# Performance work log

Hardware: AMD Instinct MI355X
Metric: run time of the kernel (lower is better)

The kernel has to match this reference:

```python
import jax, jax.numpy as jnp
import numpy as np

B, T, C = 2, 2048, 1024
NUM_HEADS, QK_LEN, V_LEN = 16, 64, 64


def setup_inputs() -> dict:
    key = jax.random.key(0)
    ks = jax.random.split(key, 11)
    s = 0.02
    return {
        "Q": jax.random.normal(ks[0], (B, T, C), jnp.float32),
        "K": jax.random.normal(ks[1], (B, T, C), jnp.float32),
        "V": jax.random.normal(ks[2], (B, T, C), jnp.float32),
        # Linear weights stored as (in, out); y = x @ W + b
        "Wq": jax.random.normal(ks[3], (C, NUM_HEADS * QK_LEN), jnp.float32) * s,
        "bq": jnp.zeros((NUM_HEADS * QK_LEN,), jnp.float32),
        "Wk": jax.random.normal(ks[4], (C, NUM_HEADS * QK_LEN), jnp.float32) * s,
        "bk": jnp.zeros((NUM_HEADS * QK_LEN,), jnp.float32),
        "Wv": jax.random.normal(ks[5], (C, NUM_HEADS * V_LEN), jnp.float32) * s,
        "bv": jnp.zeros((NUM_HEADS * V_LEN,), jnp.float32),
        "Wo": jax.random.normal(ks[6], (NUM_HEADS * V_LEN, C), jnp.float32) * s,
        "bo": jnp.zeros((C,), jnp.float32),
    }


def _split_heads(x, n_heads, d):
    b, t, _ = x.shape
    return x.reshape(b, t, n_heads, d).transpose(0, 2, 1, 3)  # (B,H,T,d)


def reference(Q, K, V, Wq, bq, Wk, bk, Wv, bv, Wo, bo):
    q = _split_heads(Q @ Wq + bq, NUM_HEADS, QK_LEN)   # (B,H,T,dk)
    k = _split_heads(K @ Wk + bk, NUM_HEADS, QK_LEN)   # (B,H,T,dk)
    v = _split_heads(V @ Wv + bv, NUM_HEADS, V_LEN)    # (B,H,T,dv)

    scale = 1.0 / jnp.sqrt(jnp.asarray(QK_LEN, q.dtype))
    scores = jnp.einsum("bhqd,bhkd->bhqk", q, k) * scale  # (B,H,T,T)
    attn = jax.nn.softmax(scores, axis=-1)
    out = jnp.einsum("bhqk,bhkd->bhqd", attn, v)           # (B,H,T,dv)

    out = out.transpose(0, 2, 1, 3).reshape(Q.shape[0], Q.shape[1], NUM_HEADS * V_LEN)
    return out @ Wo + bo
```

## Files before the change

### kernel.cpp

```cpp
#include <hip/hip_runtime.h>
#include <hip/hip_bf16.h>
#include <math.h>

constexpr int B = 2, T = 2048, C = 1024, H = 16, D = 64;
constexpr int M = B * T;
constexpr float SCALE_L2E = 0.125f * 1.4426950408889634f;

typedef __attribute__((ext_vector_type(8))) short s16x8;
typedef __attribute__((ext_vector_type(4))) short s16x4;
typedef __attribute__((ext_vector_type(4))) float fv4;

typedef unsigned short ushort_t;

static __device__ __forceinline__ ushort_t f2bf(float x) {
    union { float f; unsigned u; } c; c.f = x;
    unsigned u = c.u + 0x7FFFu + ((c.u >> 16) & 1u);
    return (ushort_t)(u >> 16);
}

#define GLDS(gp, lp) __builtin_amdgcn_global_load_lds( \
    (const __attribute__((address_space(1))) void*)(gp), \
    (__attribute__((address_space(3))) void*)(lp), 16, 0, 0)

__global__ __launch_bounds__(256) void convert_qkv(
    const float* __restrict__ Q, const float* __restrict__ K,
    const float* __restrict__ V, ushort_t* __restrict__ dst)
{
    size_t e = ((size_t)blockIdx.x * 256 + threadIdx.x) * 8;
    const float* src;
    size_t base;
    if (e < (size_t)M * C)          { src = Q; base = 0; }
    else if (e < 2 * (size_t)M * C) { src = K; base = (size_t)M * C; }
    else                            { src = V; base = 2 * (size_t)M * C; }
    const float* p = src + (e - base);
    float4 a = *(const float4*)p;
    float4 b = *(const float4*)(p + 4);
    union { s16x8 v; ushort_t u[8]; } o;
    o.u[0] = f2bf(a.x); o.u[1] = f2bf(a.y); o.u[2] = f2bf(a.z); o.u[3] = f2bf(a.w);
    o.u[4] = f2bf(b.x); o.u[5] = f2bf(b.y); o.u[6] = f2bf(b.z); o.u[7] = f2bf(b.w);
    *(s16x8*)(dst + e) = o.v;
}

__global__ __launch_bounds__(256) void transpose_w(
    const float* __restrict__ W0, const float* __restrict__ W1,
    const float* __restrict__ W2, const float* __restrict__ W3,
    ushort_t* __restrict__ Wt)
{
    const int s = blockIdx.z;
    const float* W = (s == 0) ? W0 : (s == 1) ? W1 : (s == 2) ? W2 : W3;
    const int k0 = blockIdx.x * 64, n0 = blockIdx.y * 64;
    __shared__ ushort_t tile[64][72];
    const int tid = threadIdx.x;
#pragma unroll
    for (int it = 0; it < 4; it++) {
        int f = it * 256 + tid;
        int r = f >> 4, c4 = (f & 15) * 4;
        float4 x = *(const float4*)(W + (size_t)(k0 + r) * C + n0 + c4);
        tile[r][c4 + 0] = f2bf(x.x);
        tile[r][c4 + 1] = f2bf(x.y);
        tile[r][c4 + 2] = f2bf(x.z);
        tile[r][c4 + 3] = f2bf(x.w);
    }
    __syncthreads();
#pragma unroll
    for (int it = 0; it < 4; it++) {
        int f = it * 256 + tid;
        int rr = f >> 4, c4 = (f & 15) * 4;
        union { s16x4 v; ushort_t u[4]; } u;
#pragma unroll
        for (int j = 0; j < 4; j++) u.u[j] = tile[c4 + j][rr];
        *(s16x4*)(Wt + (size_t)(s * 1024 + n0 + rr) * 1024 + k0 + c4) = u.v;
    }
}

__global__ __launch_bounds__(256) void transpose_v(
    const ushort_t* __restrict__ vw, ushort_t* __restrict__ vt)
{
    __shared__ ushort_t tile[64][72];
    const int tid = threadIdx.x;
    const int t0 = blockIdx.x * 64;
    const int bh = blockIdx.y;
    const ushort_t* src = vw + ((size_t)bh * T + t0) * D;
#pragma unroll
    for (int it = 0; it < 2; it++) {
        int f = it * 256 + tid;
        int row = f >> 3, c8 = (f & 7) * 8;
        *(s16x8*)&tile[row][c8] = *(const s16x8*)(src + (size_t)row * D + c8);
    }
    __syncthreads();
    ushort_t* dst = vt + (size_t)bh * D * T + t0;
#pragma unroll
    for (int it = 0; it < 4; it++) {
        int f = it * 256 + tid;
        int d = f >> 4, t4 = (f & 15) * 4;
        union { s16x4 v; ushort_t u[4]; } u;
#pragma unroll
        for (int j = 0; j < 4; j++) u.u[j] = tile[t4 + j][d];
        *(s16x4*)(dst + (size_t)d * T + t4) = u.v;
    }
}

__global__ __launch_bounds__(256) void gemm_qkv(
    const ushort_t* __restrict__ qkv, const ushort_t* __restrict__ Wt,
    const float* __restrict__ bq, const float* __restrict__ bk,
    const float* __restrict__ bv,
    ushort_t* __restrict__ qw, ushort_t* __restrict__ kw,
    ushort_t* __restrict__ vw)
{
    __shared__ ushort_t As[2][128 * 32];
    __shared__ ushort_t Bs[2][128 * 32];

    const int tid = threadIdx.x;
    const int w = tid >> 6, lane = tid & 63;
    const int quad = lane >> 4, lc = lane & 15;
    const int wm = w & 1, wn = w >> 1;

    const int nt = blockIdx.x;
    const int m0 = blockIdx.y * 128;
    const int s = nt >> 3;
    const int nsec0 = (nt & 7) * 128;

    const ushort_t* Abase = qkv + (size_t)s * M * C;
    const ushort_t* Btbase = Wt + (size_t)nt * 128 * 1024;

    const int srow = (w << 4) + (lane >> 2);
    const int ske  = (lane & 3) * 8;

    fv4 acc[4][4] = {};

    auto stage = [&](int k0, int buf) {
#pragma unroll
        for (int i = 0; i < 2; i++) {
            int row = i * 64 + srow;
            GLDS(Abase + (size_t)(m0 + row) * 1024 + k0 + ske,
                 As[buf] + i * 2048 + w * 512);
            GLDS(Btbase + (size_t)row * 1024 + k0 + ske,
                 Bs[buf] + i * 2048 + w * 512);
        }
    };

    stage(0, 0);
    __syncthreads();

    for (int k0 = 0; k0 < 1024; k0 += 32) {
        const int cur = (k0 >> 5) & 1;
        if (k0 + 32 < 1024) stage(k0 + 32, cur ^ 1);

        s16x8 af[4], bf[4];
#pragma unroll
        for (int ms = 0; ms < 4; ms++)
            af[ms] = *(const s16x8*)(As[cur] + (wm * 64 + ms * 16 + lc) * 32 + quad * 8);
#pragma unroll
        for (int ns = 0; ns < 4; ns++)
            bf[ns] = *(const s16x8*)(Bs[cur] + (wn * 64 + ns * 16 + lc) * 32 + quad * 8);
#pragma unroll
        for (int ms = 0; ms < 4; ms++)
#pragma unroll
            for (int ns = 0; ns < 4; ns++)
                acc[ms][ns] = __builtin_amdgcn_mfma_f32_16x16x32_bf16(
                    af[ms], bf[ns], acc[ms][ns], 0, 0, 0);
        __syncthreads();
    }

    const float* biasp = (s == 0) ? bq : (s == 1) ? bk : bv;
    const float premul = (s == 0) ? SCALE_L2E : 1.0f;
    ushort_t* outp = (s == 0) ? qw : (s == 1) ? kw : vw;

#pragma unroll
    for (int ns = 0; ns < 4; ns++) {
        const int nl = nsec0 + wn * 64 + ns * 16 + lc;
        const float bias = biasp[nl];
        const int h_ = nl >> 6, d_ = nl & 63;
#pragma unroll
        for (int ms = 0; ms < 4; ms++) {
#pragma unroll
            for (int r = 0; r < 4; r++) {
                int m = m0 + wm * 64 + ms * 16 + quad * 4 + r;
                float val = (acc[ms][ns][r] + bias) * premul;
                int b_ = m >> 11, t_ = m & (T - 1);
                size_t bh = (size_t)(b_ * H + h_);
                outp[((bh * T + t_) << 6) + d_] = f2bf(val);
            }
        }
    }
}

__global__ __launch_bounds__(256) void gemm_final(
    const ushort_t* __restrict__ A, const ushort_t* __restrict__ Wot,
    const float* __restrict__ bo, float* __restrict__ out)
{
    __shared__ ushort_t As[2][128 * 32];
    __shared__ ushort_t Bs[2][64 * 32];

    const int tid = threadIdx.x;
    const int w = tid >> 6, lane = tid & 63;
    const int quad = lane >> 4, lc = lane & 15;
    const int wm = w & 1, wn = w >> 1;

    const int n0 = blockIdx.x * 64;
    const int m0 = blockIdx.y * 128;

    const int srow = (w << 4) + (lane >> 2);
    const int ske  = (lane & 3) * 8;

    fv4 acc[4][2] = {};

    auto stage = [&](int k0, int buf) {
        GLDS(A + (size_t)(m0 + srow) * 1024 + k0 + ske,      As[buf] + w * 512);
        GLDS(A + (size_t)(m0 + 64 + srow) * 1024 + k0 + ske, As[buf] + 2048 + w * 512);
        GLDS(Wot + (size_t)(n0 + srow) * 1024 + k0 + ske,    Bs[buf] + w * 512);
    };

    stage(0, 0);
    __syncthreads();

    for (int k0 = 0; k0 < 1024; k0 += 32) {
        const int cur = (k0 >> 5) & 1;
        if (k0 + 32 < 1024) stage(k0 + 32, cur ^ 1);

        s16x8 af[4], bf[2];
#pragma unroll
        for (int ms = 0; ms < 4; ms++)
            af[ms] = *(const s16x8*)(As[cur] + (wm * 64 + ms * 16 + lc) * 32 + quad * 8);
#pragma unroll
        for (int ns = 0; ns < 2; ns++)
            bf[ns] = *(const s16x8*)(Bs[cur] + (wn * 32 + ns * 16 + lc) * 32 + quad * 8);
#pragma unroll
        for (int ms = 0; ms < 4; ms++)
#pragma unroll
            for (int ns = 0; ns < 2; ns++)
                acc[ms][ns] = __builtin_amdgcn_mfma_f32_16x16x32_bf16(
                    af[ms], bf[ns], acc[ms][ns], 0, 0, 0);
        __syncthreads();
    }

#pragma unroll
    for (int ns = 0; ns < 2; ns++) {
        const int n = n0 + wn * 32 + ns * 16 + lc;
        const float bias = bo[n];
#pragma unroll
        for (int ms = 0; ms < 4; ms++) {
#pragma unroll
            for (int r = 0; r < 4; r++) {
                int m = m0 + wm * 64 + ms * 16 + quad * 4 + r;
                out[(size_t)m * 1024 + n] = acc[ms][ns][r] + bias;
            }
        }
    }
}

__global__ __launch_bounds__(256, 4) void attn(
    const ushort_t* __restrict__ q, const ushort_t* __restrict__ k,
    const ushort_t* __restrict__ vT, ushort_t* __restrict__ o)
{
    __shared__ alignas(16) ushort_t ks[2][64 * 64];
    __shared__ alignas(16) ushort_t vs[2][64 * 64];
    __shared__ alignas(16) ushort_t ps[4 * 16 * 40];

    const int tid = threadIdx.x;
    const int w = tid >> 6, lane = tid & 63;
    const int quad = lane >> 4, lc = lane & 15;
    const int cs = lc & 7;
    const int qsub = w & 1, ksub = w >> 1;
    const int qt = blockIdx.x;
    const int bh = blockIdx.y;

    s16x8 aq[2][2];
    const ushort_t* qb = q + ((size_t)bh * T + qt * 64 + qsub * 32) * D;
#pragma unroll
    for (int j = 0; j < 2; j++)
#pragma unroll
        for (int h = 0; h < 2; h++)
            aq[j][h] = *(const s16x8*)(qb + (size_t)(j * 16 + lc) * D + h * 32 + quad * 8);

    fv4 accO[2][4] = {};
    float psum[2] = {0.f, 0.f};

    const ushort_t* kb0 = k + (size_t)bh * T * D;
    const ushort_t* vb0 = vT + (size_t)bh * D * T;

    const int sr8 = lane >> 3;
    const int sch = (lane & 7) ^ sr8;

    auto stage = [&](int kt, int buf) {
#pragma unroll
        for (int i = 0; i < 2; i++) {
            const int r = w * 16 + i * 8 + sr8;
            GLDS(kb0 + (size_t)(kt * 64 + r) * 64 + sch * 8,
                 ks[buf] + (w * 16 + i * 8) * 64);
            GLDS(vb0 + (size_t)r * T + kt * 64 + sch * 8,
                 vs[buf] + (w * 16 + i * 8) * 64);
        }
    };

    stage(0, 0);
    __syncthreads();

    ushort_t* psw = ps + (w * 16) * 40;

    for (int kt = 0; kt < T / 64; kt++) {
        const int cur = kt & 1;
        if (kt + 1 < T / 64) stage(kt + 1, cur ^ 1);

        fv4 accST[2][2] = {};
#pragma unroll
        for (int t4k = 0; t4k < 2; t4k++) {
            const int row = ksub * 32 + t4k * 16 + lc;
            s16x8 ak0 = *(const s16x8*)(ks[cur] + row * 64 + ((quad ^ cs) << 3));
            s16x8 ak1 = *(const s16x8*)(ks[cur] + row * 64 + (((quad + 4) ^ cs) << 3));
#pragma unroll
            for (int j = 0; j < 2; j++) {
                accST[j][t4k] = __builtin_amdgcn_mfma_f32_16x16x32_bf16(
                    ak0, aq[j][0], accST[j][t4k], 0, 0, 0);
                accST[j][t4k] = __builtin_amdgcn_mfma_f32_16x16x32_bf16(
                    ak1, aq[j][1], accST[j][t4k], 0, 0, 0);
            }
        }

        s16x8 av[4];
#pragma unroll
        for (int t4v = 0; t4v < 4; t4v++) {
            const int row = t4v * 16 + lc;
            av[t4v] = *(const s16x8*)(vs[cur] + row * 64 + (((ksub * 4 + quad) ^ cs) << 3));
        }

#pragma unroll
        for (int j = 0; j < 2; j++) {
            float c0 = 0.f, c1 = 0.f;
#pragma unroll
            for (int t4k = 0; t4k < 2; t4k++) {
                union { s16x4 v; ushort_t u[4]; } pk;
                float p0 = __builtin_amdgcn_exp2f(accST[j][t4k][0]);
                float p1 = __builtin_amdgcn_exp2f(accST[j][t4k][1]);
                float p2 = __builtin_amdgcn_exp2f(accST[j][t4k][2]);
                float p3 = __builtin_amdgcn_exp2f(accST[j][t4k][3]);
                pk.u[0] = f2bf(p0); pk.u[1] = f2bf(p1);
                pk.u[2] = f2bf(p2); pk.u[3] = f2bf(p3);
                if (t4k == 0) c0 = (p0 + p1) + (p2 + p3);
                else          c1 = (p0 + p1) + (p2 + p3);
                *(s16x4*)(psw + lc * 40 + t4k * 16 + quad * 4) = pk.v;
            }
            psum[j] += c0 + c1;

            s16x8 pb = *(const s16x8*)(psw + lc * 40 + quad * 8);
#pragma unroll
            for (int t4v = 0; t4v < 4; t4v++)
                accO[j][t4v] = __builtin_amdgcn_mfma_f32_16x16x32_bf16(
                    av[t4v], pb, accO[j][t4v], 0, 0, 0);
        }

        __syncthreads();
    }

#pragma unroll
    for (int j = 0; j < 2; j++) {
        psum[j] += __shfl_xor(psum[j], 16);
        psum[j] += __shfl_xor(psum[j], 32);
    }

    float* sc = (float*)ps;
#pragma unroll
    for (int c = 0; c < 4; c++) {
        const int j = c >> 1, tv = (c & 1) * 2;
        __syncthreads();
        if (ksub == 1) {
            *(fv4*)(sc + ((qsub * 64 + lane) * 8))     = accO[j][tv];
            *(fv4*)(sc + ((qsub * 64 + lane) * 8 + 4)) = accO[j][tv + 1];
        }
        __syncthreads();
        if (ksub == 0) {
            accO[j][tv]     += *(fv4*)(sc + ((qsub * 64 + lane) * 8));
            accO[j][tv + 1] += *(fv4*)(sc + ((qsub * 64 + lane) * 8 + 4));
        }
    }
    __syncthreads();
    if (ksub == 1) {
        sc[(qsub * 64 + lane) * 2]     = psum[0];
        sc[(qsub * 64 + lane) * 2 + 1] = psum[1];
    }
    __syncthreads();
    if (ksub == 0) {
        psum[0] += sc[(qsub * 64 + lane) * 2];
        psum[1] += sc[(qsub * 64 + lane) * 2 + 1];

        const int b_ = bh >> 4, h_ = bh & 15;
#pragma unroll
        for (int j = 0; j < 2; j++) {
            float inv = 1.0f / psum[j];
            int row = qt * 64 + qsub * 32 + j * 16 + lc;
            ushort_t* op = o + ((size_t)b_ * T + row) * C + h_ * 64;
#pragma unroll
            for (int t4v = 0; t4v < 4; t4v++) {
                union { s16x4 v; ushort_t u[4]; } u;
#pragma unroll
                for (int r = 0; r < 4; r++) u.u[r] = f2bf(accO[j][t4v][r] * inv);
                *(s16x4*)(op + t4v * 16 + quad * 4) = u.v;
            }
        }
    }
}

extern "C" void kernel_launch(void* const* d_in, const int* in_sizes, int n_in,
                              void* d_out, int out_size, void* d_ws, size_t ws_size,
                              hipStream_t stream)
{
    const float* Q  = (const float*)d_in[0];
    const float* K  = (const float*)d_in[1];
    const float* V  = (const float*)d_in[2];
    const float* Wq = (const float*)d_in[3];
    const float* bq = (const float*)d_in[4];
    const float* Wk = (const float*)d_in[5];
    const float* bk = (const float*)d_in[6];
    const float* Wv = (const float*)d_in[7];
    const float* bv = (const float*)d_in[8];
    const float* Wo = (const float*)d_in[9];
    const float* bo = (const float*)d_in[10];
    float* out = (float*)d_out;

    ushort_t* qkvbf = (ushort_t*)d_ws;
    ushort_t* Wt = qkvbf + (size_t)3 * M * C;
    ushort_t* qw = Wt + (size_t)4096 * 1024;
    ushort_t* kw = qw + (size_t)M * C;
    ushort_t* vw = kw + (size_t)M * C;
    ushort_t* vt = vw + (size_t)M * C;
    ushort_t* ow = qkvbf;
    ushort_t* Wot = Wt + (size_t)3072 * 1024;

    dim3 blk(256);
    convert_qkv<<<dim3(3 * M * C / 2048), blk, 0, stream>>>(Q, K, V, qkvbf);
    transpose_w<<<dim3(16, 16, 4), blk, 0, stream>>>(Wq, Wk, Wv, Wo, Wt);
    gemm_qkv<<<dim3(24, 32), blk, 0, stream>>>(qkvbf, Wt, bq, bk, bv, qw, kw, vw);
    transpose_v<<<dim3(T / 64, B * H), blk, 0, stream>>>(vw, vt);
    attn<<<dim3(T / 64, B * H), blk, 0, stream>>>(qw, kw, vt, ow);
    gemm_final<<<dim3(16, 32), blk, 0, stream>>>(ow, Wot, bo, out);
}
```

Before: 243.5 us.

## Use hardware bf16 packing, in-register P shuffle, MFMA priority and block swizzle

Replaces the software round-to-nearest bf16 conversion with the packed v_cvt_pk_bf16_f32 instruction in the convert, weight-transpose and attention kernels. The attention kernel no longer stages P through LDS: it reorders the packed probabilities across lanes with permlane32/permlane16 swaps to build the MFMA operand directly, removing an LDS round trip per tile. It also raises wave priority around the MFMA blocks and remaps block indices so neighbouring blocks work on different heads. The lane-permutation layout must exactly match the previous LDS transpose, and the remapped grid order changes cache locality.

Result: faster. 235.7 us (-3.2%).

```diff
diff --git a/kernel.cpp b/kernel.cpp
--- a/kernel.cpp
+++ b/kernel.cpp
@@ -16,6 +16,12 @@
     union { float f; unsigned u; } c; c.f = x;
     unsigned u = c.u + 0x7FFFu + ((c.u >> 16) & 1u);
     return (ushort_t)(u >> 16);
+}
+
+static __device__ __forceinline__ int cvt_pk_bf16(float lo, float hi) {
+    int r;
+    asm("v_cvt_pk_bf16_f32 %0, %1, %2" : "=v"(r) : "v"(lo), "v"(hi));
+    return r;
 }
 
 #define GLDS(gp, lp) __builtin_amdgcn_global_load_lds( \
@@ -35,9 +41,11 @@
     const float* p = src + (e - base);
     float4 a = *(const float4*)p;
     float4 b = *(const float4*)(p + 4);
-    union { s16x8 v; ushort_t u[8]; } o;
-    o.u[0] = f2bf(a.x); o.u[1] = f2bf(a.y); o.u[2] = f2bf(a.z); o.u[3] = f2bf(a.w);
-    o.u[4] = f2bf(b.x); o.u[5] = f2bf(b.y); o.u[6] = f2bf(b.z); o.u[7] = f2bf(b.w);
+    union { s16x8 v; int i[4]; } o;
+    o.i[0] = cvt_pk_bf16(a.x, a.y);
+    o.i[1] = cvt_pk_bf16(a.z, a.w);
+    o.i[2] = cvt_pk_bf16(b.x, b.y);
+    o.i[3] = cvt_pk_bf16(b.z, b.w);
     *(s16x8*)(dst + e) = o.v;
 }
 
@@ -56,10 +64,8 @@
         int f = it * 256 + tid;
         int r = f >> 4, c4 = (f & 15) * 4;
         float4 x = *(const float4*)(W + (size_t)(k0 + r) * C + n0 + c4);
-        tile[r][c4 + 0] = f2bf(x.x);
-        tile[r][c4 + 1] = f2bf(x.y);
-        tile[r][c4 + 2] = f2bf(x.z);
-        tile[r][c4 + 3] = f2bf(x.w);
+        *(int*)&tile[r][c4]     = cvt_pk_bf16(x.x, x.y);
+        *(int*)&tile[r][c4 + 2] = cvt_pk_bf16(x.z, x.w);
     }
     __syncthreads();
 #pragma unroll
@@ -255,15 +261,16 @@
 {
     __shared__ alignas(16) ushort_t ks[2][64 * 64];
     __shared__ alignas(16) ushort_t vs[2][64 * 64];
-    __shared__ alignas(16) ushort_t ps[4 * 16 * 40];
 
     const int tid = threadIdx.x;
     const int w = tid >> 6, lane = tid & 63;
     const int quad = lane >> 4, lc = lane & 15;
     const int cs = lc & 7;
     const int qsub = w & 1, ksub = w >> 1;
-    const int qt = blockIdx.x;
-    const int bh = blockIdx.y;
+
+    const int id = blockIdx.y * 32 + blockIdx.x;
+    const int qt = (id >> 3) & 31;
+    const int bh = (id & 7) * 4 + (id >> 8);
 
     s16x8 aq[2][2];
     const ushort_t* qb = q + ((size_t)bh * T + qt * 64 + qsub * 32) * D;
@@ -296,13 +303,12 @@
     stage(0, 0);
     __syncthreads();
 
-    ushort_t* psw = ps + (w * 16) * 40;
-
     for (int kt = 0; kt < T / 64; kt++) {
         const int cur = kt & 1;
         if (kt + 1 < T / 64) stage(kt + 1, cur ^ 1);
 
         fv4 accST[2][2] = {};
+        __builtin_amdgcn_s_setprio(1);
 #pragma unroll
         for (int t4k = 0; t4k < 2; t4k++) {
             const int row = ksub * 32 + t4k * 16 + lc;
@@ -316,6 +322,7 @@
                     ak1, aq[j][1], accST[j][t4k], 0, 0, 0);
             }
         }
+        __builtin_amdgcn_s_setprio(0);
 
         s16x8 av[4];
 #pragma unroll
@@ -326,27 +333,34 @@
 
 #pragma unroll
         for (int j = 0; j < 2; j++) {
-            float c0 = 0.f, c1 = 0.f;
-#pragma unroll
-            for (int t4k = 0; t4k < 2; t4k++) {
-                union { s16x4 v; ushort_t u[4]; } pk;
-                float p0 = __builtin_amdgcn_exp2f(accST[j][t4k][0]);
-                float p1 = __builtin_amdgcn_exp2f(accST[j][t4k][1]);
-                float p2 = __builtin_amdgcn_exp2f(accST[j][t4k][2]);
-                float p3 = __builtin_amdgcn_exp2f(accST[j][t4k][3]);
-                pk.u[0] = f2bf(p0); pk.u[1] = f2bf(p1);
-                pk.u[2] = f2bf(p2); pk.u[3] = f2bf(p3);
-                if (t4k == 0) c0 = (p0 + p1) + (p2 + p3);
-                else          c1 = (p0 + p1) + (p2 + p3);
-                *(s16x4*)(psw + lc * 40 + t4k * 16 + quad * 4) = pk.v;
-            }
-            psum[j] += c0 + c1;
-
-            s16x8 pb = *(const s16x8*)(psw + lc * 40 + quad * 8);
+            float p0 = __builtin_amdgcn_exp2f(accST[j][0][0]);
+            float p1 = __builtin_amdgcn_exp2f(accST[j][0][1]);
+            float p2 = __builtin_amdgcn_exp2f(accST[j][0][2]);
+            float p3 = __builtin_amdgcn_exp2f(accST[j][0][3]);
+            float p4 = __builtin_amdgcn_exp2f(accST[j][1][0]);
+            float p5 = __builtin_amdgcn_exp2f(accST[j][1][1]);
+            float p6 = __builtin_amdgcn_exp2f(accST[j][1][2]);
+            float p7 = __builtin_amdgcn_exp2f(accST[j][1][3]);
+            psum[j] += ((p0 + p1) + (p2 + p3)) + ((p4 + p5) + (p6 + p7));
+
+            int W00 = cvt_pk_bf16(p0, p1);
+            int W01 = cvt_pk_bf16(p2, p3);
+            int W10 = cvt_pk_bf16(p4, p5);
+            int W11 = cvt_pk_bf16(p6, p7);
+            asm("v_permlane32_swap_b32 %0, %1" : "+v"(W00), "+v"(W10));
+            asm("v_permlane16_swap_b32 %0, %1" : "+v"(W00), "+v"(W10));
+            asm("v_permlane32_swap_b32 %0, %1" : "+v"(W01), "+v"(W11));
+            asm("v_permlane16_swap_b32 %0, %1" : "+v"(W01), "+v"(W11));
+
+            union { int i[4]; s16x8 v; } pbu;
+            pbu.i[0] = W00; pbu.i[1] = W01; pbu.i[2] = W10; pbu.i[3] = W11;
+
+            __builtin_amdgcn_s_setprio(1);
 #pragma unroll
             for (int t4v = 0; t4v < 4; t4v++)
                 accO[j][t4v] = __builtin_amdgcn_mfma_f32_16x16x32_bf16(
-                    av[t4v], pb, accO[j][t4v], 0, 0, 0);
+                    av[t4v], pbu.v, accO[j][t4v], 0, 0, 0);
+            __builtin_amdgcn_s_setprio(0);
         }
 
         __syncthreads();
@@ -358,7 +372,7 @@
         psum[j] += __shfl_xor(psum[j], 32);
     }
 
-    float* sc = (float*)ps;
+    float* sc = (float*)&ks[0][0];
 #pragma unroll
     for (int c = 0; c < 4; c++) {
         const int j = c >> 1, tv = (c & 1) * 2;
@@ -391,9 +405,9 @@
             ushort_t* op = o + ((size_t)b_ * T + row) * C + h_ * 64;
 #pragma unroll
             for (int t4v = 0; t4v < 4; t4v++) {
-                union { s16x4 v; ushort_t u[4]; } u;
-#pragma unroll
-                for (int r = 0; r < 4; r++) u.u[r] = f2bf(accO[j][t4v][r] * inv);
+                union { s16x4 v; int i[2]; } u;
+                u.i[0] = cvt_pk_bf16(accO[j][t4v][0] * inv, accO[j][t4v][1] * inv);
+                u.i[1] = cvt_pk_bf16(accO[j][t4v][2] * inv, accO[j][t4v][3] * inv);
                 *(s16x4*)(op + t4v * 16 + quad * 4) = u.v;
             }
         }
```
